# Optimization experiments

Hardware: AMD Instinct MI355X
Metric: run time of the kernel (lower is better)

Reference implementation:

```python
import jax, jax.numpy as jnp
import numpy as np
import math

NH = 16  # n_head
HS = 64  # head_size = n_embd // n_head


def setup_inputs() -> dict:
    key = jax.random.key(0)
    ks = jax.random.split(key, 7)
    B, T, C, QL, KVL = 2, 2048, 1024, 128, 128
    s = lambda k, shape, fan_in: jax.random.normal(k, shape, jnp.float32) / np.sqrt(fan_in)
    return {
        "x": jax.random.normal(ks[0], (B, T, C), jnp.float32),
        "W_dq": s(ks[1], (QL, C), C),
        "W_uq": s(ks[2], (C, QL), QL),
        "W_dkv": s(ks[3], (KVL, C), C),
        "W_uk": s(ks[4], (C, KVL), KVL),
        "W_uv": s(ks[5], (C, KVL), KVL),
        "W_o": s(ks[6], (C, C), C),
    }


def reference(x, W_dq, W_uq, W_dkv, W_uk, W_uv, W_o):
    B, T, C = x.shape
    kvl = W_dkv.shape[0]
    # absorbed matrices (training branch)
    k_eff = (W_dq.T @ W_uq.T @ W_uk).reshape(NH, HS, kvl)            # (nh, hs, kvl)
    v_eff = (W_uv.T @ W_o.T).reshape(kvl, NH, HS).transpose(1, 0, 2)  # (nh, kvl, hs)
    # latent kv cache
    c_kv = x @ W_dkv.T                                                # (B, T, kvl)
    # query path
    q = (x @ W_dq.T @ W_uq.T).reshape(B, T, NH, HS).transpose(0, 2, 1, 3)  # (B, nh, T, hs)
    # scores: q @ k_eff @ c_kv^T
    ql = jnp.einsum('bhtd,hdl->bhtl', q, k_eff)                       # (B, nh, T, kvl)
    scores = jnp.einsum('bhtl,bsl->bhts', ql, c_kv) / math.sqrt(HS)   # (B, nh, T, T)
    # causal mask
    mask = jnp.tril(jnp.ones((T, T), dtype=bool))
    scores = jnp.where(mask[None, None], scores, -jnp.inf)
    attn = jax.nn.softmax(scores, axis=-1)
    # output: attn @ c_kv @ v_eff
    ctx = jnp.einsum('bhts,bsl->bhtl', attn, c_kv)                    # (B, nh, T, kvl)
    y = jnp.einsum('bhtl,hld->bhtd', ctx, v_eff)                      # (B, nh, T, hs)
    y = y.transpose(0, 2, 1, 3).reshape(B, T, C)
    return y, c_kv
```

## Files before the change

kernel.cpp:

```cpp
#include <hip/hip_runtime.h>
#include <hip/hip_bf16.h>

typedef __hip_bfloat16 bf16;
typedef __attribute__((ext_vector_type(8))) short short8;
typedef __attribute__((ext_vector_type(4))) float f32x4;

#define NHD 16
#define HSD 64
#define KVLD 128
#define QLD 128
#define CD 1024
#define BD 2
#define TD 2048

__device__ __forceinline__ short8 ld8(const bf16* p) { return *(const short8*)p; }
__device__ __forceinline__ void st8(bf16* p, short8 v) { *(short8*)p = v; }

__device__ __forceinline__ void st4(bf16* p, float4 a) {
    union { short4 s; bf16 h[4]; } u;
    u.h[0] = __float2bfloat16(a.x); u.h[1] = __float2bfloat16(a.y);
    u.h[2] = __float2bfloat16(a.z); u.h[3] = __float2bfloat16(a.w);
    *(short4*)p = u.s;
}
__device__ __forceinline__ void st4f(bf16* p, f32x4 a) {
    union { short4 s; bf16 h[4]; } u;
    u.h[0] = __float2bfloat16(a[0]); u.h[1] = __float2bfloat16(a[1]);
    u.h[2] = __float2bfloat16(a[2]); u.h[3] = __float2bfloat16(a[3]);
    *(short4*)p = u.s;
}

__global__ __launch_bounds__(256) void k_pre(const float* __restrict__ wuq,
                                             const float* __restrict__ wuk,
                                             const float* __restrict__ wdq,
                                             const float* __restrict__ wdkv,
                                             float* __restrict__ m1p,
                                             float* __restrict__ G,
                                             bf16* __restrict__ wqkv_bf) {
    const int b = blockIdx.x;
    const int tid = threadIdx.x;
    if (b < 128) {
        const int part = b >> 4, ig = b & 15;
        const int i = ig * 8 + (tid >> 5);
        const int j4 = (tid & 31) << 2;
        const float* wq = wuq + (size_t)part * 128 * QLD;
        const float* wk = wuk + (size_t)part * 128 * KVLD;
        float4 acc = make_float4(0.f, 0.f, 0.f, 0.f);
        for (int c0 = 0; c0 < 128; c0 += 8) {
            float a[8]; float4 kv[8];
#pragma unroll
            for (int u = 0; u < 8; ++u) {
                a[u] = wq[(c0 + u) * QLD + i];
                kv[u] = *(const float4*)(wk + (c0 + u) * KVLD + j4);
            }
#pragma unroll
            for (int u = 0; u < 8; ++u) {
                acc.x = fmaf(a[u], kv[u].x, acc.x);
                acc.y = fmaf(a[u], kv[u].y, acc.y);
                acc.z = fmaf(a[u], kv[u].z, acc.z);
                acc.w = fmaf(a[u], kv[u].w, acc.w);
            }
        }
        *(float4*)(m1p + (size_t)part * 16384 + (size_t)i * 128 + j4) = acc;
    } else if (b < 256) {
        const int b1 = b - 128;
        const int h = b1 >> 3, p8 = b1 & 7;
        const int p = p8 * 16 + (tid >> 4);
        const int i8 = (tid & 15) << 3;
        float acc[8];
#pragma unroll
        for (int t = 0; t < 8; ++t) acc[t] = 0.f;
        const float* wdqp = wdq + (size_t)p * CD + h * 64;
        const float* wuqh = wuq + (size_t)(h * 64) * QLD + i8;
        for (int d0 = 0; d0 < 64; d0 += 8) {
            float a[8]; float4 b0[8], b1v[8];
#pragma unroll
            for (int u = 0; u < 8; ++u) {
                a[u] = wdqp[d0 + u];
                b0[u] = *(const float4*)(wuqh + (d0 + u) * QLD);
                b1v[u] = *(const float4*)(wuqh + (d0 + u) * QLD + 4);
            }
#pragma unroll
            for (int u = 0; u < 8; ++u) {
                acc[0] = fmaf(a[u], b0[u].x, acc[0]);  acc[1] = fmaf(a[u], b0[u].y, acc[1]);
                acc[2] = fmaf(a[u], b0[u].z, acc[2]);  acc[3] = fmaf(a[u], b0[u].w, acc[3]);
                acc[4] = fmaf(a[u], b1v[u].x, acc[4]); acc[5] = fmaf(a[u], b1v[u].y, acc[5]);
                acc[6] = fmaf(a[u], b1v[u].z, acc[6]); acc[7] = fmaf(a[u], b1v[u].w, acc[7]);
            }
        }
        float* dst = G + (size_t)h * 16384 + (size_t)p * 128 + i8;
        *(float4*)dst = make_float4(acc[0], acc[1], acc[2], acc[3]);
        *(float4*)(dst + 4) = make_float4(acc[4], acc[5], acc[6], acc[7]);
    } else {
        const int r = (b - 256) * 4 + (tid >> 6);
        const int lane = tid & 63;
        const float* src = (r < 128) ? (wdq + (size_t)r * CD) : (wdkv + (size_t)(r - 128) * CD);
        float4 f[4];
#pragma unroll
        for (int k = 0; k < 4; ++k) f[k] = ((const float4*)src)[lane + k * 64];
#pragma unroll
        for (int k = 0; k < 4; ++k)
            st4(wqkv_bf + (size_t)r * CD + (lane + k * 64) * 4, f[k]);
    }
}

__global__ __launch_bounds__(256) void k_main(const float* __restrict__ x,
                                              const bf16* __restrict__ wqkv_bf,
                                              const float* __restrict__ m1p,
                                              const float* __restrict__ G,
                                              const float* __restrict__ wuv,
                                              const float* __restrict__ wo,
                                              bf16* __restrict__ q1_bf,
                                              float* __restrict__ ckv_out,
                                              bf16* __restrict__ ckv_bf,
                                              bf16* __restrict__ ckvT_bf,
                                              bf16* __restrict__ Et_bf,
                                              bf16* __restrict__ veffT_bf) {
    __shared__ __align__(16) char arena[49152];
    const int blk = blockIdx.x;
    const int tid = threadIdx.x;

    if (blk < 256) {
        const int m0 = blk * 16;
        const int w = tid >> 6, lane = tid & 63, m16 = lane & 15, g = lane >> 4;
        bf16* As = (bf16*)arena;
        bf16* Bs = (bf16*)(arena + 2304);

        const int arow = tid >> 4, akc = (tid & 15) << 2;
        const float* axp = x + (size_t)(m0 + arow) * CD + akc;
        int brow[8], bkc[8];
#pragma unroll
        for (int kk = 0; kk < 8; ++kk) {
            int v = tid + kk * 256;
            brow[kk] = v >> 3; bkc[kk] = (v & 7) << 3;
        }

        float4 pA = *(const float4*)(axp);
        short8 pB[8];
#pragma unroll
        for (int kk = 0; kk < 8; ++kk)
            pB[kk] = ld8(wqkv_bf + (size_t)brow[kk] * CD + bkc[kk]);

        f32x4 acc[4];
#pragma unroll
        for (int nb = 0; nb < 4; ++nb) acc[nb] = (f32x4){0.f, 0.f, 0.f, 0.f};

        for (int k0 = 0; k0 < CD; k0 += 64) {
            __syncthreads();
            st4(As + arow * 72 + akc, pA);
#pragma unroll
            for (int kk = 0; kk < 8; ++kk)
                st8(Bs + brow[kk] * 72 + bkc[kk], pB[kk]);
            __syncthreads();
            if (k0 + 64 < CD) {
                pA = *(const float4*)(axp + k0 + 64);
#pragma unroll
                for (int kk = 0; kk < 8; ++kk)
                    pB[kk] = ld8(wqkv_bf + (size_t)brow[kk] * CD + k0 + 64 + bkc[kk]);
            }
            short8 aF[2];
#pragma unroll
            for (int kf = 0; kf < 2; ++kf)
                aF[kf] = ld8(As + m16 * 72 + kf * 32 + g * 8);
#pragma unroll
            for (int nb = 0; nb < 4; ++nb)
#pragma unroll
                for (int kf = 0; kf < 2; ++kf) {
                    short8 bF = ld8(Bs + (w * 64 + nb * 16 + m16) * 72 + kf * 32 + g * 8);
                    acc[nb] = __builtin_amdgcn_mfma_f32_16x16x32_bf16(aF[kf], bF, acc[nb], 0, 0, 0);
                }
        }

#pragma unroll
        for (int nb = 0; nb < 4; ++nb)
#pragma unroll
            for (int r = 0; r < 4; ++r) {
                int t = m0 + g * 4 + r;
                int col = w * 64 + nb * 16 + m16;
                float v = acc[nb][r];
                if (col < 128) {
                    q1_bf[(size_t)t * QLD + col] = __float2bfloat16(v);
                } else {
                    int l = col - 128;
                    ckv_out[(size_t)t * KVLD + l] = v;
                    bf16 hv = __float2bfloat16(v);
                    ckv_bf[(size_t)t * KVLD + l] = hv;
                    int b = t >> 11, tl = t & 2047;
                    ckvT_bf[((size_t)b * KVLD + l) * TD + tl] = hv;
                }
            }
    } else if (blk < 512) {
        const int b2 = blk - 256;
        const int h = b2 >> 4, lb = b2 & 15;
        float* m1s = (float*)arena;
        for (int v = tid; v < 1024; v += 256) {
            int p = v >> 3, lq = v & 7;
            float s0 = 0.f;
            float t0[8];
#pragma unroll
            for (int part = 0; part < 8; ++part)
                t0[part] = m1p[(size_t)part * 16384 + (size_t)p * 128 + lb * 8 + lq];
#pragma unroll
            for (int part = 0; part < 8; ++part) s0 += t0[part];
            m1s[v] = s0;
        }
        __syncthreads();
        const int lq = tid >> 5, i4 = (tid & 31) << 2;
        const float* Gh = G + (size_t)h * 16384;
        float4 acc = make_float4(0.f, 0.f, 0.f, 0.f);
        for (int p0 = 0; p0 < 128; p0 += 8) {
            float4 g[8]; float a[8];
#pragma unroll
            for (int u = 0; u < 8; ++u) {
                g[u] = *(const float4*)(Gh + (p0 + u) * 128 + i4);
                a[u] = m1s[(p0 + u) * 8 + lq];
            }
#pragma unroll
            for (int u = 0; u < 8; ++u) {
                acc.x = fmaf(a[u], g[u].x, acc.x);
                acc.y = fmaf(a[u], g[u].y, acc.y);
                acc.z = fmaf(a[u], g[u].z, acc.z);
                acc.w = fmaf(a[u], g[u].w, acc.w);
            }
        }
        const float sc = 0.1803368801f;
        const int l = lb * 8 + lq;
        st4(Et_bf + ((size_t)h * 128 + l) * 128 + i4,
            make_float4(sc * acc.x, sc * acc.y, sc * acc.z, sc * acc.w));
    } else {
        const int b3 = blk - 512;
        const int cc0 = b3 * 4;
        float* woS = (float*)arena;
        float* wuvS = (float*)arena + 4096;
#pragma unroll
        for (int k = 0; k < 4; ++k)
            ((float4*)woS)[tid + k * 256] = ((const float4*)(wo + (size_t)cc0 * CD))[tid + k * 256];

        const int r = tid >> 6;
        const int lh = tid & 63;
        float4 pf[8];
#pragma unroll
        for (int t = 0; t < 8; ++t)
            pf[t] = ((const float4*)wuv)[t * 256 + tid];

        float a0 = 0.f, a1 = 0.f;
        for (int ch = 0; ch < 16; ++ch) {
            __syncthreads();
#pragma unroll
            for (int t = 0; t < 8; ++t)
                ((float4*)wuvS)[t * 256 + tid] = pf[t];
            __syncthreads();
            if (ch < 15) {
#pragma unroll
                for (int t = 0; t < 8; ++t)
                    pf[t] = ((const float4*)wuv)[(ch + 1) * 2048 + t * 256 + tid];
            }
            const float* wr = woS + r * 1024 + ch * 64;
            const float2* vv = (const float2*)wuvS + lh;
            for (int cb = 0; cb < 64; cb += 8) {
                float wv[8]; float2 v[8];
#pragma unroll
                for (int u = 0; u < 8; ++u) {
                    wv[u] = wr[cb + u];
                    v[u] = vv[(cb + u) * 64];
                }
#pragma unroll
                for (int u = 0; u < 8; ++u) {
                    a0 = fmaf(wv[u], v[u].x, a0);
                    a1 = fmaf(wv[u], v[u].y, a1);
                }
            }
        }
        union { short2 s; bf16 h2[2]; } u;
        u.h2[0] = __float2bfloat16(a0);
        u.h2[1] = __float2bfloat16(a1);
        *(short2*)(veffT_bf + (size_t)(cc0 + r) * KVLD + lh * 2) = u.s;
    }
}

__global__ __launch_bounds__(512, 4) void k_flash(const bf16* __restrict__ Q1_bf,
                                                  const bf16* __restrict__ Et_bf,
                                                  const bf16* __restrict__ ckv_bf,
                                                  const bf16* __restrict__ ckvT_bf,
                                                  const bf16* __restrict__ veffT_bf,
                                                  float* __restrict__ yout) {
    const int h = blockIdx.x & 15;
    const int b = blockIdx.x >> 4;
    const int qlo = blockIdx.y;
    const int qhi = 31 - qlo;
    const int tid = threadIdx.x;
    const int w = tid >> 6;
    const int ws = w >> 2;
    const int wq = w & 3;
    const int lane = tid & 63;
    const int m16 = lane & 15;
    const int g = lane >> 4;
    const int myqt = ws ? qlo : qhi;
    const int row0 = myqt * 64;

    __shared__ __align__(16) short smem_raw[28288];
    bf16* smem = (bf16*)smem_raw;
    bf16* kvN = smem;
    bf16* kvT = smem + 8704;
    bf16* pS  = smem + 19072 + w * 1152;
    bf16* bufLo = kvT;
    bf16* vT = smem + 19072;

    {
        const bf16 one = __float2bfloat16(1.0f);
        for (int idx = tid; idx < 16 * 72; idx += 512)
            kvT[9216 + idx] = one;
    }

    {
        const bf16* q1hi = Q1_bf + ((size_t)(b * TD + qhi * 64)) * QLD;
        const bf16* q1lo = Q1_bf + ((size_t)(b * TD + qlo * 64)) * QLD;
#pragma unroll
        for (int k = 0; k < 2; ++k) {
            int v = tid + k * 512;
            int row = v >> 4, cv = (v & 15) << 3;
            st8(kvN + row * 136 + cv, ld8(q1hi + row * QLD + cv));
            st8(bufLo + row * 136 + cv, ld8(q1lo + row * QLD + cv));
        }
    }
    __syncthreads();
    bf16* myQ1 = ws ? bufLo : kvN;
    {
        short8 aq[4];
#pragma unroll
        for (int kf = 0; kf < 4; ++kf)
            aq[kf] = ld8(myQ1 + (wq * 16 + m16) * 136 + kf * 32 + g * 8);
        const bf16* Eh = Et_bf + (size_t)h * QLD * KVLD;
        f32x4 qc[8];
#pragma unroll
        for (int nb = 0; nb < 8; ++nb) qc[nb] = (f32x4){0.f, 0.f, 0.f, 0.f};
#pragma unroll
        for (int nb = 0; nb < 8; ++nb)
#pragma unroll
            for (int kf = 0; kf < 4; ++kf) {
                short8 bq = ld8(Eh + (nb * 16 + m16) * QLD + kf * 32 + g * 8);
                qc[nb] = __builtin_amdgcn_mfma_f32_16x16x32_bf16(aq[kf], bq, qc[nb], 0, 0, 0);
            }
        __syncthreads();
#pragma unroll
        for (int nb = 0; nb < 8; ++nb)
#pragma unroll
            for (int r = 0; r < 4; ++r)
                myQ1[(wq * 16 + g * 4 + r) * 136 + nb * 16 + m16] = __float2bfloat16(qc[nb][r]);
    }
    __syncthreads();
    short8 qlA[4];
#pragma unroll
    for (int kf = 0; kf < 4; ++kf)
        qlA[kf] = ld8(myQ1 + (wq * 16 + m16) * 136 + kf * 32 + g * 8);

    f32x4 cx[9];
#pragma unroll
    for (int nb = 0; nb < 9; ++nb) cx[nb] = (f32x4){0.f, 0.f, 0.f, 0.f};
    float mrow = -INFINITY;
    const int rg = row0 + wq * 16 + m16;

    const bf16* ckb = ckv_bf + (size_t)b * TD * KVLD;
    const bf16* ckTb = ckvT_bf + (size_t)b * KVLD * TD;

    int nrow[2], ncol[2], trow[2], tcol[2];
#pragma unroll
    for (int k = 0; k < 2; ++k) {
        int v = tid + k * 512;
        nrow[k] = v >> 4; ncol[k] = (v & 15) << 3;
        trow[k] = v >> 3; tcol[k] = (v & 7) << 3;
    }
    short8 pfN[2], pfT[2];
#pragma unroll
    for (int k = 0; k < 2; ++k) {
        pfN[k] = ld8(ckb + (size_t)nrow[k] * KVLD + ncol[k]);
        pfT[k] = ld8(ckTb + (size_t)trow[k] * TD + tcol[k]);
    }

    for (int tile = 0; tile <= qhi; ++tile) {
        const int s0 = tile * 64;
        __syncthreads();
#pragma unroll
        for (int k = 0; k < 2; ++k) {
            st8(kvN + nrow[k] * 136 + ncol[k], pfN[k]);
            st8(kvT + trow[k] * 72 + tcol[k], pfT[k]);
        }
        __syncthreads();
        if (tile < qhi) {
            const int s1 = s0 + 64;
#pragma unroll
            for (int k = 0; k < 2; ++k) {
                pfN[k] = ld8(ckb + (size_t)(s1 + nrow[k]) * KVLD + ncol[k]);
                pfT[k] = ld8(ckTb + (size_t)trow[k] * TD + s1 + tcol[k]);
            }
        }

        if (ws == 0 || tile <= qlo) {
            f32x4 sa[4];
#pragma unroll
            for (int nb = 0; nb < 4; ++nb) sa[nb] = (f32x4){0.f, 0.f, 0.f, 0.f};
#pragma unroll
            for (int nb = 0; nb < 4; ++nb)
#pragma unroll
                for (int kf = 0; kf < 4; ++kf) {
                    short8 ak = ld8(kvN + (nb * 16 + m16) * 136 + kf * 32 + g * 8);
                    sa[nb] = __builtin_amdgcn_mfma_f32_16x16x32_bf16(ak, qlA[kf], sa[nb], 0, 0, 0);
                }

            if (tile == myqt) {
#pragma unroll
                for (int nb = 0; nb < 4; ++nb)
#pragma unroll
                    for (int r = 0; r < 4; ++r) {
                        int sg = s0 + nb * 16 + g * 4 + r;
                        if (sg > rg) sa[nb][r] = -INFINITY;
                    }
            }

            float mloc = sa[0][0];
#pragma unroll
            for (int nb = 0; nb < 4; ++nb)
#pragma unroll
                for (int r = 0; r < 4; ++r) mloc = fmaxf(mloc, sa[nb][r]);
            mloc = fmaxf(mloc, __shfl_xor(mloc, 16));
            mloc = fmaxf(mloc, __shfl_xor(mloc, 32));
            if (__any(mloc > mrow)) {
                float mt = fmaxf(mrow, mloc);
                float al = exp2f(mrow - mt);
                mrow = mt;
#pragma unroll
                for (int nb = 0; nb < 9; ++nb)
#pragma unroll
                    for (int r = 0; r < 4; ++r) cx[nb][r] *= al;
            }

#pragma unroll
            for (int nb = 0; nb < 4; ++nb) {
                float4 p4;
                p4.x = exp2f(sa[nb][0] - mrow);
                p4.y = exp2f(sa[nb][1] - mrow);
                p4.z = exp2f(sa[nb][2] - mrow);
                p4.w = exp2f(sa[nb][3] - mrow);
                st4(pS + m16 * 72 + nb * 16 + g * 4, p4);
            }
            __builtin_amdgcn_wave_barrier();

            short8 pA[2];
#pragma unroll
            for (int kf = 0; kf < 2; ++kf)
                pA[kf] = ld8(pS + m16 * 72 + kf * 32 + g * 8);
#pragma unroll
            for (int nb = 0; nb < 9; ++nb)
#pragma unroll
                for (int kf = 0; kf < 2; ++kf) {
                    short8 av = ld8(kvT + (nb * 16 + m16) * 72 + kf * 32 + g * 8);
                    cx[nb] = __builtin_amdgcn_mfma_f32_16x16x32_bf16(av, pA[kf], cx[nb], 0, 0, 0);
                }
        }
    }

    float invl = 1.f / cx[8][0];
#pragma unroll
    for (int nb = 0; nb < 8; ++nb)
#pragma unroll
        for (int r = 0; r < 4; ++r) cx[nb][r] *= invl;
    __syncthreads();
    bf16* ctxS = ws ? bufLo : kvN;
#pragma unroll
    for (int nb = 0; nb < 8; ++nb)
        st4f(ctxS + (wq * 16 + m16) * 136 + nb * 16 + g * 4, cx[nb]);
    {
        const bf16* vsrc = veffT_bf + (size_t)h * HSD * KVLD;
#pragma unroll
        for (int k = 0; k < 2; ++k) {
            int v = tid + k * 512;
            int row = v >> 4, cv = (v & 15) << 3;
            st8(vT + row * 136 + cv, ld8(vsrc + row * KVLD + cv));
        }
    }
    __syncthreads();

    short8 cB[4];
#pragma unroll
    for (int kf = 0; kf < 4; ++kf)
        cB[kf] = ld8(ctxS + (wq * 16 + m16) * 136 + kf * 32 + g * 8);
    f32x4 ya[4];
#pragma unroll
    for (int nb = 0; nb < 4; ++nb) ya[nb] = (f32x4){0.f, 0.f, 0.f, 0.f};
#pragma unroll
    for (int nb = 0; nb < 4; ++nb)
#pragma unroll
        for (int kf = 0; kf < 4; ++kf) {
            short8 av = ld8(vT + (nb * 16 + m16) * 136 + kf * 32 + g * 8);
            ya[nb] = __builtin_amdgcn_mfma_f32_16x16x32_bf16(av, cB[kf], ya[nb], 0, 0, 0);
        }
    float* yo = yout + ((size_t)b * TD + rg) * CD + h * HSD;
#pragma unroll
    for (int nb = 0; nb < 4; ++nb)
        *(float4*)(yo + nb * 16 + g * 4) = *(float4*)&ya[nb];
}

extern "C" void kernel_launch(void* const* d_in, const int* in_sizes, int n_in,
                              void* d_out, int out_size, void* d_ws, size_t ws_size,
                              hipStream_t stream) {
    const float* x    = (const float*)d_in[0];
    const float* wdq  = (const float*)d_in[1];
    const float* wuq  = (const float*)d_in[2];
    const float* wdkv = (const float*)d_in[3];
    const float* wuk  = (const float*)d_in[4];
    const float* wuv  = (const float*)d_in[5];
    const float* wo   = (const float*)d_in[6];
    float* yout = (float*)d_out;
    float* ckv_out = yout + (size_t)BD * TD * CD;

    float* ws = (float*)d_ws;
    float* M1P = ws;
    float* G   = M1P + 131072;
    bf16* wqkv_bf  = (bf16*)(G + 262144);
    bf16* Et_bf    = wqkv_bf + 262144;
    bf16* veffT_bf = Et_bf + 262144;
    bf16* ckv_bf   = veffT_bf + 131072;
    bf16* ckvT_bf  = ckv_bf + 524288;
    bf16* Q1_bf    = ckvT_bf + 524288;

    k_pre <<<320, 256, 0, stream>>>(wuq, wuk, wdq, wdkv, M1P, G, wqkv_bf);
    k_main<<<768, 256, 0, stream>>>(x, wqkv_bf, M1P, G, wuv, wo,
                                    Q1_bf, ckv_out, ckv_bf, ckvT_bf, Et_bf, veffT_bf);

    dim3 grid(32, 16);
    k_flash<<<grid, 512, 0, stream>>>(Q1_bf, Et_bf, ckv_bf, ckvT_bf, veffT_bf, yout);
}
```

Baseline: 225.4 us.

## Fuse weight bf16 conversion into projection GEMM and lazily rescale softmax max

The separate k_pre pass that converted W_dq/W_dkv to bf16 is removed; the k_main projection GEMM now loads fp32 weights and converts them in registers before staging them to shared memory. The Q1 MFMA operands are swapped so each lane writes four contiguous bf16 values with a vector store instead of scattered scalar stores. The online softmax now rescales only when the new row max exceeds the running max by more than 8 (in log2 units), which skips most rescale passes but lets exponentials grow up to 2^8 before correction. The fused load doubles global weight traffic per GEMM tile and adds conversion work inside the loop.

```diff
diff --git a/kernel.cpp b/kernel.cpp
--- a/kernel.cpp
+++ b/kernel.cpp
@@ -16,6 +16,14 @@
 __device__ __forceinline__ short8 ld8(const bf16* p) { return *(const short8*)p; }
 __device__ __forceinline__ void st8(bf16* p, short8 v) { *(short8*)p = v; }
 
+__device__ __forceinline__ short8 cvt8(float4 a, float4 b) {
+    union { short8 s; bf16 h[8]; } u;
+    u.h[0] = __float2bfloat16(a.x); u.h[1] = __float2bfloat16(a.y);
+    u.h[2] = __float2bfloat16(a.z); u.h[3] = __float2bfloat16(a.w);
+    u.h[4] = __float2bfloat16(b.x); u.h[5] = __float2bfloat16(b.y);
+    u.h[6] = __float2bfloat16(b.z); u.h[7] = __float2bfloat16(b.w);
+    return u.s;
+}
 __device__ __forceinline__ void st4(bf16* p, float4 a) {
     union { short4 s; bf16 h[4]; } u;
     u.h[0] = __float2bfloat16(a.x); u.h[1] = __float2bfloat16(a.y);
@@ -32,10 +40,8 @@
 __global__ __launch_bounds__(256) void k_pre(const float* __restrict__ wuq,
                                              const float* __restrict__ wuk,
                                              const float* __restrict__ wdq,
-                                             const float* __restrict__ wdkv,
                                              float* __restrict__ m1p,
-                                             float* __restrict__ G,
-                                             bf16* __restrict__ wqkv_bf) {
+                                             float* __restrict__ G) {
     const int b = blockIdx.x;
     const int tid = threadIdx.x;
     if (b < 128) {
@@ -61,7 +67,7 @@
             }
         }
         *(float4*)(m1p + (size_t)part * 16384 + (size_t)i * 128 + j4) = acc;
-    } else if (b < 256) {
+    } else {
         const int b1 = b - 128;
         const int h = b1 >> 3, p8 = b1 & 7;
         const int p = p8 * 16 + (tid >> 4);
@@ -90,21 +96,12 @@
         float* dst = G + (size_t)h * 16384 + (size_t)p * 128 + i8;
         *(float4*)dst = make_float4(acc[0], acc[1], acc[2], acc[3]);
         *(float4*)(dst + 4) = make_float4(acc[4], acc[5], acc[6], acc[7]);
-    } else {
-        const int r = (b - 256) * 4 + (tid >> 6);
-        const int lane = tid & 63;
-        const float* src = (r < 128) ? (wdq + (size_t)r * CD) : (wdkv + (size_t)(r - 128) * CD);
-        float4 f[4];
-#pragma unroll
-        for (int k = 0; k < 4; ++k) f[k] = ((const float4*)src)[lane + k * 64];
-#pragma unroll
-        for (int k = 0; k < 4; ++k)
-            st4(wqkv_bf + (size_t)r * CD + (lane + k * 64) * 4, f[k]);
     }
 }
 
 __global__ __launch_bounds__(256) void k_main(const float* __restrict__ x,
-                                              const bf16* __restrict__ wqkv_bf,
+                                              const float* __restrict__ wdq,
+                                              const float* __restrict__ wdkv,
                                               const float* __restrict__ m1p,
                                               const float* __restrict__ G,
                                               const float* __restrict__ wuv,
@@ -128,17 +125,22 @@
         const int arow = tid >> 4, akc = (tid & 15) << 2;
         const float* axp = x + (size_t)(m0 + arow) * CD + akc;
         int brow[8], bkc[8];
+        const float* bsrc[8];
 #pragma unroll
         for (int kk = 0; kk < 8; ++kk) {
             int v = tid + kk * 256;
             brow[kk] = v >> 3; bkc[kk] = (v & 7) << 3;
+            bsrc[kk] = ((brow[kk] < 128) ? (wdq + (size_t)brow[kk] * CD)
+                                         : (wdkv + (size_t)(brow[kk] - 128) * CD)) + bkc[kk];
         }
 
         float4 pA = *(const float4*)(axp);
-        short8 pB[8];
-#pragma unroll
-        for (int kk = 0; kk < 8; ++kk)
-            pB[kk] = ld8(wqkv_bf + (size_t)brow[kk] * CD + bkc[kk]);
+        float4 pB0[8], pB1[8];
+#pragma unroll
+        for (int kk = 0; kk < 8; ++kk) {
+            pB0[kk] = *(const float4*)(bsrc[kk]);
+            pB1[kk] = *(const float4*)(bsrc[kk] + 4);
+        }
 
         f32x4 acc[4];
 #pragma unroll
@@ -149,13 +151,15 @@
             st4(As + arow * 72 + akc, pA);
 #pragma unroll
             for (int kk = 0; kk < 8; ++kk)
-                st8(Bs + brow[kk] * 72 + bkc[kk], pB[kk]);
+                st8(Bs + brow[kk] * 72 + bkc[kk], cvt8(pB0[kk], pB1[kk]));
             __syncthreads();
             if (k0 + 64 < CD) {
                 pA = *(const float4*)(axp + k0 + 64);
 #pragma unroll
-                for (int kk = 0; kk < 8; ++kk)
-                    pB[kk] = ld8(wqkv_bf + (size_t)brow[kk] * CD + k0 + 64 + bkc[kk]);
+                for (int kk = 0; kk < 8; ++kk) {
+                    pB0[kk] = *(const float4*)(bsrc[kk] + k0 + 64);
+                    pB1[kk] = *(const float4*)(bsrc[kk] + k0 + 68);
+                }
             }
             short8 aF[2];
 #pragma unroll
@@ -194,11 +198,11 @@
         float* m1s = (float*)arena;
         for (int v = tid; v < 1024; v += 256) {
             int p = v >> 3, lq = v & 7;
-            float s0 = 0.f;
             float t0[8];
 #pragma unroll
             for (int part = 0; part < 8; ++part)
                 t0[part] = m1p[(size_t)part * 16384 + (size_t)p * 128 + lb * 8 + lq];
+            float s0 = 0.f;
 #pragma unroll
             for (int part = 0; part < 8; ++part) s0 += t0[part];
             m1s[v] = s0;
@@ -338,14 +342,12 @@
 #pragma unroll
             for (int kf = 0; kf < 4; ++kf) {
                 short8 bq = ld8(Eh + (nb * 16 + m16) * QLD + kf * 32 + g * 8);
-                qc[nb] = __builtin_amdgcn_mfma_f32_16x16x32_bf16(aq[kf], bq, qc[nb], 0, 0, 0);
+                qc[nb] = __builtin_amdgcn_mfma_f32_16x16x32_bf16(bq, aq[kf], qc[nb], 0, 0, 0);
             }
         __syncthreads();
 #pragma unroll
         for (int nb = 0; nb < 8; ++nb)
-#pragma unroll
-            for (int r = 0; r < 4; ++r)
-                myQ1[(wq * 16 + g * 4 + r) * 136 + nb * 16 + m16] = __float2bfloat16(qc[nb][r]);
+            st4f(myQ1 + (wq * 16 + m16) * 136 + nb * 16 + g * 4, qc[nb]);
     }
     __syncthreads();
     short8 qlA[4];
@@ -423,7 +425,7 @@
                 for (int r = 0; r < 4; ++r) mloc = fmaxf(mloc, sa[nb][r]);
             mloc = fmaxf(mloc, __shfl_xor(mloc, 16));
             mloc = fmaxf(mloc, __shfl_xor(mloc, 32));
-            if (__any(mloc > mrow)) {
+            if (__any(mloc > mrow + 8.f)) {
                 float mt = fmaxf(mrow, mloc);
                 float al = exp2f(mrow - mt);
                 mrow = mt;
@@ -515,15 +517,14 @@
     float* ws = (float*)d_ws;
     float* M1P = ws;
     float* G   = M1P + 131072;
-    bf16* wqkv_bf  = (bf16*)(G + 262144);
-    bf16* Et_bf    = wqkv_bf + 262144;
+    bf16* Et_bf    = (bf16*)(G + 262144);
     bf16* veffT_bf = Et_bf + 262144;
     bf16* ckv_bf   = veffT_bf + 131072;
     bf16* ckvT_bf  = ckv_bf + 524288;
     bf16* Q1_bf    = ckvT_bf + 524288;
 
-    k_pre <<<320, 256, 0, stream>>>(wuq, wuk, wdq, wdkv, M1P, G, wqkv_bf);
-    k_main<<<768, 256, 0, stream>>>(x, wqkv_bf, M1P, G, wuv, wo,
+    k_pre <<<256, 256, 0, stream>>>(wuq, wuk, wdq, M1P, G);
+    k_main<<<768, 256, 0, stream>>>(x, wdq, wdkv, M1P, G, wuv, wo,
                                     Q1_bf, ckv_out, ckv_bf, ckvT_bf, Et_bf, veffT_bf);
 
     dim3 grid(32, 16);
```

Measured after the change: 246.4 us. 1.09x slower.
